# Performance work log

Hardware: AMD Instinct MI355X
Metric: run time of the kernel (lower is better)

## Reference

```python
import jax, jax.numpy as jnp
import numpy as np

D_MODEL = 1024
NUM_HEADS = 16
DEPTH = D_MODEL // NUM_HEADS
B, S = 4, 1024


def setup_inputs() -> dict:
    key = jax.random.key(0)
    ks = jax.random.split(key, 12)
    sc = 1.0 / np.sqrt(D_MODEL)
    return {
        "v": jax.random.normal(ks[0], (B, S, D_MODEL), jnp.float32),
        "k": jax.random.normal(ks[1], (B, S, D_MODEL), jnp.float32),
        "q": jax.random.normal(ks[2], (B, S, D_MODEL), jnp.float32),
        "mask": jnp.zeros((B, 1, 1, S), jnp.float32),
        "adjoin_matrix": jax.random.normal(ks[3], (B, 1, S, S), jnp.float32),
        "wq_w": jax.random.normal(ks[4], (D_MODEL, D_MODEL), jnp.float32) * sc,
        "wq_b": jnp.zeros((D_MODEL,), jnp.float32),
        "wk_w": jax.random.normal(ks[5], (D_MODEL, D_MODEL), jnp.float32) * sc,
        "wk_b": jnp.zeros((D_MODEL,), jnp.float32),
        "wv_w": jax.random.normal(ks[6], (D_MODEL, D_MODEL), jnp.float32) * sc,
        "wv_b": jnp.zeros((D_MODEL,), jnp.float32),
        "dense_w": jax.random.normal(ks[7], (D_MODEL, D_MODEL), jnp.float32) * sc,
        "dense_b": jnp.zeros((D_MODEL,), jnp.float32),
    }


def _split_heads(x, batch):
    # [B, S, D] -> [B, H, S, depth]
    return x.reshape(batch, -1, NUM_HEADS, DEPTH).transpose(0, 2, 1, 3)


def reference(v, k, q, mask, adjoin_matrix,
              wq_w, wq_b, wk_w, wk_b, wv_w, wv_b, dense_w, dense_b):
    batch = q.shape[0]
    # torch nn.Linear: y = x @ W^T + b
    qh = _split_heads(q @ wq_w.T + wq_b, batch)
    kh = _split_heads(k @ wk_w.T + wk_b, batch)
    vh = _split_heads(v @ wv_w.T + wv_b, batch)

    logits = jnp.einsum('bhqd,bhkd->bhqk', qh, kh) / jnp.sqrt(
        jnp.asarray(DEPTH, qh.dtype))
    logits = logits + mask * (-1e9) + adjoin_matrix
    attn = jax.nn.softmax(logits, axis=-1).astype(qh.dtype)
    # dropout p=0 -> identity at inference
    ctx = jnp.einsum('bhqk,bhkd->bhqd', attn, vh)  # [B,H,S,depth]
    concat = ctx.transpose(0, 2, 1, 3).reshape(batch, -1, D_MODEL)
    out = concat @ dense_w.T + dense_b
    return out, attn
```

## Files before the change

kernel.cpp:

```cpp
#include <hip/hip_runtime.h>
#include <hip/hip_bf16.h>
#include <cstdint>
#include <cstddef>

#define B_ 4
#define S_ 1024
#define D_ 1024
#define H_ 16
#define DEPTH_ 64
#define M_ (B_*S_)

typedef __attribute__((ext_vector_type(4))) float f32x4;
typedef __attribute__((ext_vector_type(8))) __bf16 bf16x8;
typedef __attribute__((ext_vector_type(8))) unsigned short u16x8;
typedef __attribute__((ext_vector_type(4))) unsigned short u16x4;

typedef const __attribute__((address_space(1))) unsigned int GU32;
typedef __attribute__((address_space(3))) unsigned int LU32;

__device__ __forceinline__ unsigned short f2bf(float f) {
  unsigned int u = __builtin_bit_cast(unsigned int, f);
  u += 0x7FFFu + ((u >> 16) & 1u);
  return (unsigned short)(u >> 16);
}

__device__ __forceinline__ float bf2f(unsigned short v) {
  unsigned int u = (unsigned int)v << 16;
  return __builtin_bit_cast(float, u);
}

struct CvtAll { const float* s[7]; unsigned short* d[7]; };

__device__ __forceinline__ void cvt_body(const float* __restrict__ s,
                                         unsigned short* __restrict__ d, int i) {
  const f32x4* sp = (const f32x4*)s + (size_t)i * 2;
  f32x4 a = sp[0], b = sp[1];
  u16x8 o;
  o[0]=f2bf(a[0]); o[1]=f2bf(a[1]); o[2]=f2bf(a[2]); o[3]=f2bf(a[3]);
  o[4]=f2bf(b[0]); o[5]=f2bf(b[1]); o[6]=f2bf(b[2]); o[7]=f2bf(b[3]);
  *((u16x8*)d + i) = o;
}

__global__ void cvt_all_kernel(CvtAll a) {
  int bi = blockIdx.x, seg, i;
  if (bi < 6144) { seg = bi >> 11;              i = ((bi & 2047) << 8) + threadIdx.x; }
  else           { int t = bi - 6144; seg = 3 + (t >> 9); i = ((t & 511) << 8) + threadIdx.x; }
  cvt_body(a.s[seg], a.d[seg], i);
}

__device__ __forceinline__ void gemm_body(
    const unsigned short* __restrict__ A,
    const unsigned short* __restrict__ Bm,
    unsigned short* __restrict__ Obf,
    float* __restrict__ Of32,
    const float* __restrict__ bias,
    int N, int K, float scale, int biasRow, int m0, int n0)
{
  __shared__ unsigned short As[128*32];
  __shared__ unsigned short Bs[128*32];
  const int tid  = threadIdx.x;
  const int lane = tid & 63;
  const int w    = tid >> 6;
  const int wm   = w >> 1, wn = w & 1;
  const int fr   = lane & 15, kg = lane >> 4;

  f32x4 acc[4][4];
  #pragma unroll
  for (int i = 0; i < 4; ++i)
    #pragma unroll
    for (int j = 0; j < 4; ++j)
      acc[i][j] = (f32x4)0.0f;

  const int o0 = tid * 16,        o1 = (256 + tid) * 16;
  const int r0 = o0 >> 6,         c0 = (o0 & 63) >> 1;
  const int r1 = o1 >> 6,         c1 = (o1 & 63) >> 1;
  const int lds0 = (w * 64) * 16;
  const int lds1 = (256 + w * 64) * 16;

  const int nkt = K >> 5;
  for (int kt = 0; kt < nkt; ++kt) {
    const int kk = kt * 32;
    __builtin_amdgcn_global_load_lds((GU32*)(A  + (size_t)(m0 + r0) * K + kk + c0),
                                     (LU32*)((char*)As + lds0), 16, 0, 0);
    __builtin_amdgcn_global_load_lds((GU32*)(A  + (size_t)(m0 + r1) * K + kk + c1),
                                     (LU32*)((char*)As + lds1), 16, 0, 0);
    __builtin_amdgcn_global_load_lds((GU32*)(Bm + (size_t)(n0 + r0) * K + kk + c0),
                                     (LU32*)((char*)Bs + lds0), 16, 0, 0);
    __builtin_amdgcn_global_load_lds((GU32*)(Bm + (size_t)(n0 + r1) * K + kk + c1),
                                     (LU32*)((char*)Bs + lds1), 16, 0, 0);
    __syncthreads();

    bf16x8 af[4], bf[4];
    #pragma unroll
    for (int i = 0; i < 4; ++i)
      af[i] = *(const bf16x8*)&As[(wm * 64 + i * 16 + fr) * 32 + kg * 8];
    #pragma unroll
    for (int j = 0; j < 4; ++j)
      bf[j] = *(const bf16x8*)&Bs[(wn * 64 + j * 16 + fr) * 32 + kg * 8];
    #pragma unroll
    for (int i = 0; i < 4; ++i)
      #pragma unroll
      for (int j = 0; j < 4; ++j)
        acc[i][j] = __builtin_amdgcn_mfma_f32_16x16x32_bf16(af[i], bf[j], acc[i][j], 0, 0, 0);
    __syncthreads();
  }

  #pragma unroll
  for (int i = 0; i < 4; ++i) {
    const int rowb = m0 + wm * 64 + i * 16 + kg * 4;
    #pragma unroll
    for (int j = 0; j < 4; ++j) {
      const int col = n0 + wn * 64 + j * 16 + fr;
      const float bcol = biasRow ? 0.0f : bias[col];
      #pragma unroll
      for (int r = 0; r < 4; ++r) {
        const int row = rowb + r;
        const float bv = biasRow ? bias[row] : bcol;
        const float val = (acc[i][j][r] + bv) * scale;
        if (Obf) Obf[(size_t)row * N + col] = f2bf(val);
        else     Of32[(size_t)row * N + col] = val;
      }
    }
  }
}

struct GemmSet { const unsigned short* A; const unsigned short* Bm;
                 unsigned short* O; const float* bias; };

__launch_bounds__(256)
__global__ void qkv_gemm(GemmSet s0, GemmSet s1, GemmSet s2) {
  const int z = blockIdx.y;
  GemmSet s = (z == 0) ? s0 : (z == 1) ? s1 : s2;
  int m0, n0, N; float scale; int biasRow;
  if (z < 2) { m0 = (blockIdx.x & 31) * 128; n0 = (blockIdx.x >> 5) * 128;
               N = D_; scale = (z == 0) ? 0.125f : 1.0f; biasRow = 0; }
  else       { m0 = (blockIdx.x & 7) * 128;  n0 = (blockIdx.x >> 3) * 128;
               N = M_; scale = 1.0f; biasRow = 1; }
  gemm_body(s.A, s.Bm, s.O, nullptr, s.bias, N, D_, scale, biasRow, m0, n0);
}

__launch_bounds__(256)
__global__ void dense_gemm(const unsigned short* __restrict__ A,
                           const unsigned short* __restrict__ Bm,
                           float* __restrict__ O, const float* __restrict__ bias) {
  gemm_body(A, Bm, nullptr, O, bias, D_, D_, 1.0f, 0,
            blockIdx.x * 128, blockIdx.y * 128);
}

__launch_bounds__(512, 2)
__global__ void attn_kernel(const unsigned short* __restrict__ qp,
                            const unsigned short* __restrict__ kp,
                            const unsigned short* __restrict__ vt,
                            const float* __restrict__ mask,
                            const float* __restrict__ adjoin,
                            float* __restrict__ attn_out,
                            unsigned short* __restrict__ ctx)
{
  __shared__ __align__(16) char L[136192];
  char* const Pb  = L;
  char* const Mbb = L + 65536;
  float* const ssum = (float*)(L + 69632);

  const int tid = threadIdx.x, lane = tid & 63, w = tid >> 6;
  const int fr = lane & 15, kg = lane >> 4;
  const int fm = w >> 2, fd = w & 3;
  const int frsw = (fr & 7) << 4;
  const int r8 = lane >> 3;
  const int c7p = (((lane & 7) ^ r8) << 4);

  char* const Wb  = L + 70656 + w * 8192;
  char* const Ks0 = Wb,        * const Ks1 = Wb + 2048;
  char* const As0 = Wb + 4096, * const As1 = Wb + 6144;

  const int i_ = blockIdx.x;
  const int bh = (i_ & 7) * 8 + ((i_ >> 3) & 7);
  const int qt = i_ >> 6;
  const int b = bh >> 4, h = bh & 15;
  const int q0 = qt * 32;
  const int kw = w * 128;

  const char* kG = (const char*)(kp + (size_t)b * S_ * D_ + h * DEPTH_);
  const char* aG = (const char*)(adjoin + (size_t)b * S_ * S_ + (size_t)q0 * S_);
  const char* vG = (const char*)(vt + (size_t)h * DEPTH_ * M_ + (size_t)b * S_);
  const char* mG = (const char*)(mask + (size_t)b * S_);

  auto stageK = [&](int t, char* dst) {
    #pragma unroll
    for (int j = 0; j < 2; ++j)
      __builtin_amdgcn_global_load_lds(
          (GU32*)(kG + (size_t)(kw + t * 16 + j * 8 + r8) * 2048 + c7p),
          (LU32*)(dst + j * 1024 + lane * 16), 16, 0, 0);
  };
  auto stageA = [&](int t, char* dst) {
    #pragma unroll
    for (int j = 0; j < 2; ++j) {
      const int qA = j * 8 + r8 + ((c7p >> 6) << 4);
      __builtin_amdgcn_global_load_lds(
          (GU32*)(aG + (size_t)qA * 4096 + kw * 4 + t * 64 + (c7p & 63)),
          (LU32*)(dst + j * 1024 + lane * 16), 16, 0, 0);
    }
  };
  auto stageV = [&](int t, char* dst) {
    #pragma unroll
    for (int j = 0; j < 2; ++j)
      __builtin_amdgcn_global_load_lds(
          (GU32*)(vG + (size_t)(fd * 16 + j * 8 + r8) * 8192 + t * 128 + c7p),
          (LU32*)(dst + j * 1024 + lane * 16), 16, 0, 0);
  };

  const unsigned short* q0p = qp + ((size_t)b * S_ + q0 + fr) * D_ + h * DEPTH_;
  const unsigned short* q1p = q0p + 16 * D_;
  bf16x8 qf00 = *(const bf16x8*)&q0p[kg * 8];
  bf16x8 qf01 = *(const bf16x8*)&q0p[32 + kg * 8];
  bf16x8 qf10 = *(const bf16x8*)&q1p[kg * 8];
  bf16x8 qf11 = *(const bf16x8*)&q1p[32 + kg * 8];

  if (w < 4)
    __builtin_amdgcn_global_load_lds((GU32*)(mG + (w << 10) + lane * 16),
                                     (LU32*)(Mbb + (w << 10) + lane * 16), 16, 0, 0);
  stageK(0, Ks0); stageA(0, As0);
  stageK(1, Ks1); stageA(1, As1);
  asm volatile("s_waitcnt vmcnt(4)" ::: "memory");
  __builtin_amdgcn_s_barrier();
  __builtin_amdgcn_sched_barrier(0);

  float ls0 = 0.0f, ls1 = 0.0f;

  #pragma unroll
  for (int t = 0; t < 8; ++t) {
    if (t == 7) asm volatile("s_waitcnt vmcnt(2)" ::: "memory");
    else        asm volatile("s_waitcnt vmcnt(4)" ::: "memory");
    __builtin_amdgcn_sched_barrier(0);

    const char* kb = (t & 1) ? Ks1 : Ks0;
    const char* ab = (t & 1) ? As1 : As0;
    bf16x8 kf0 = *(const bf16x8*)(kb + fr * 128 + ((kg * 16) ^ frsw));
    bf16x8 kf1 = *(const bf16x8*)(kb + fr * 128 + ((64 + kg * 16) ^ frsw));
    f32x4 a40 = *(const f32x4*)(ab + fr * 128 + ((kg * 16) ^ frsw));
    f32x4 a41 = *(const f32x4*)(ab + fr * 128 + ((64 + kg * 16) ^ frsw));
    f32x4 m4  = *(const f32x4*)(Mbb + kw * 4 + t * 64 + kg * 16);

    asm volatile("s_waitcnt lgkmcnt(0)" ::: "memory");
    __builtin_amdgcn_sched_barrier(0);

    if (t < 6)      { stageK(t + 2, (t & 1) ? Ks1 : Ks0);
                      stageA(t + 2, (t & 1) ? As1 : As0); }
    else if (t == 6)  stageV(0, As0);
    else              stageV(1, As1);

    f32x4 s0 = (f32x4)0.0f, s1 = (f32x4)0.0f;
    s0 = __builtin_amdgcn_mfma_f32_16x16x32_bf16(kf0, qf00, s0, 0, 0, 0);
    s0 = __builtin_amdgcn_mfma_f32_16x16x32_bf16(kf1, qf01, s0, 0, 0, 0);
    s1 = __builtin_amdgcn_mfma_f32_16x16x32_bf16(kf0, qf10, s1, 0, 0, 0);
    s1 = __builtin_amdgcn_mfma_f32_16x16x32_bf16(kf1, qf11, s1, 0, 0, 0);

    f32x4 p0, p1;
    #pragma unroll
    for (int r = 0; r < 4; ++r) {
      p0[r] = __expf(s0[r] + a40[r] + m4[r] * (-1e9f));
      p1[r] = __expf(s1[r] + a41[r] + m4[r] * (-1e9f));
    }
    ls0 += (p0[0] + p0[1]) + (p0[2] + p0[3]);
    ls1 += (p1[0] + p1[1]) + (p1[2] + p1[3]);
    u16x4 pk0, pk1;
    #pragma unroll
    for (int r = 0; r < 4; ++r) { pk0[r] = f2bf(p0[r]); pk1[r] = f2bf(p1[r]); }
    const int pcol = (kw * 2 + t * 32 + kg * 8) ^ frsw;
    *(u16x4*)(Pb + fr * 2048 + pcol)        = pk0;
    *(u16x4*)(Pb + (16 + fr) * 2048 + pcol) = pk1;
  }

  ls0 += __shfl_xor(ls0, 16); ls0 += __shfl_xor(ls0, 32);
  ls1 += __shfl_xor(ls1, 16); ls1 += __shfl_xor(ls1, 32);
  if (lane < 16) {
    ssum[lane * 8 + w]        = ls0;
    ssum[(16 + lane) * 8 + w] = ls1;
  }

  asm volatile("s_waitcnt lgkmcnt(0)" ::: "memory");
  __builtin_amdgcn_s_barrier();
  __builtin_amdgcn_sched_barrier(0);

  const int q = fm * 16 + fr;
  f32x4 cacc = (f32x4)0.0f;
  #pragma unroll
  for (int t = 0; t < 16; ++t) {
    if (t == 15) asm volatile("s_waitcnt vmcnt(0)" ::: "memory");
    else         asm volatile("s_waitcnt vmcnt(2)" ::: "memory");
    __builtin_amdgcn_sched_barrier(0);

    const char* vb = (t & 1) ? As1 : As0;
    bf16x8 vf0 = *(const bf16x8*)(vb + fr * 128 + ((kg * 16) ^ frsw));
    bf16x8 vf1 = *(const bf16x8*)(vb + fr * 128 + ((64 + kg * 16) ^ frsw));
    bf16x8 pf0 = *(const bf16x8*)(Pb + q * 2048 + ((t * 128 + kg * 16) ^ frsw));
    bf16x8 pf1 = *(const bf16x8*)(Pb + q * 2048 + ((t * 128 + 64 + kg * 16) ^ frsw));

    asm volatile("s_waitcnt lgkmcnt(0)" ::: "memory");
    __builtin_amdgcn_sched_barrier(0);

    if (t < 14) stageV(t + 2, (t & 1) ? As1 : As0);

    cacc = __builtin_amdgcn_mfma_f32_16x16x32_bf16(vf0, pf0, cacc, 0, 0, 0);
    cacc = __builtin_amdgcn_mfma_f32_16x16x32_bf16(vf1, pf1, cacc, 0, 0, 0);
  }

  {
    f32x4 sa = *(const f32x4*)&ssum[q * 8];
    f32x4 sb = *(const f32x4*)&ssum[q * 8 + 4];
    const float giC = 1.0f / ((sa[0] + sa[1]) + (sa[2] + sa[3]) +
                              ((sb[0] + sb[1]) + (sb[2] + sb[3])));
    u16x4 cv;
    #pragma unroll
    for (int r = 0; r < 4; ++r) cv[r] = f2bf(cacc[r] * giC);
    *(u16x4*)&ctx[((size_t)b * S_ + q0 + q) * D_ + h * DEPTH_ + fd * 16 + kg * 4] = cv;
  }

  #pragma unroll
  for (int j = 0; j < 4; ++j) {
    const int row = w * 4 + j;
    f32x4 ta = *(const f32x4*)&ssum[row * 8];
    f32x4 tb = *(const f32x4*)&ssum[row * 8 + 4];
    const float g = 1.0f / ((ta[0] + ta[1]) + (ta[2] + ta[3]) +
                            ((tb[0] + tb[1]) + (tb[2] + tb[3])));
    const char* pr = Pb + row * 2048;
    const int rs = (row & 7) << 4;
    float* ao = attn_out + ((size_t)bh * S_ + q0 + row) * S_;
    #pragma unroll
    for (int half = 0; half < 2; ++half) {
      u16x8 pv = *(const u16x8*)(pr + ((half * 1024 + lane * 16) ^ rs));
      f32x4 o0, o1;
      #pragma unroll
      for (int e = 0; e < 4; ++e) { o0[e] = bf2f(pv[e]) * g; o1[e] = bf2f(pv[4 + e]) * g; }
      __builtin_nontemporal_store(o0, (f32x4*)(ao + half * 512 + lane * 8));
      __builtin_nontemporal_store(o1, (f32x4*)(ao + half * 512 + lane * 8 + 4));
    }
  }
}

extern "C" void kernel_launch(void* const* d_in, const int* in_sizes, int n_in,
                              void* d_out, int out_size, void* d_ws, size_t ws_size,
                              hipStream_t stream)
{
  const float* v_in   = (const float*)d_in[0];
  const float* k_in   = (const float*)d_in[1];
  const float* q_in   = (const float*)d_in[2];
  const float* mask   = (const float*)d_in[3];
  const float* adjoin = (const float*)d_in[4];
  const float* wq_w   = (const float*)d_in[5];
  const float* wq_b   = (const float*)d_in[6];
  const float* wk_w   = (const float*)d_in[7];
  const float* wk_b   = (const float*)d_in[8];
  const float* wv_w   = (const float*)d_in[9];
  const float* wv_b   = (const float*)d_in[10];
  const float* wd_w   = (const float*)d_in[11];
  const float* wd_b   = (const float*)d_in[12];

  unsigned short* xq  = (unsigned short*)d_ws;
  unsigned short* xk  = xq  + (size_t)M_ * D_;
  unsigned short* xv  = xk  + (size_t)M_ * D_;
  unsigned short* wqb = xv  + (size_t)M_ * D_;
  unsigned short* wkb = wqb + (size_t)D_ * D_;
  unsigned short* wvb = wkb + (size_t)D_ * D_;
  unsigned short* wdb = wvb + (size_t)D_ * D_;
  unsigned short* qp  = wdb + (size_t)D_ * D_;
  unsigned short* kp  = qp  + (size_t)M_ * D_;
  unsigned short* vt  = kp  + (size_t)M_ * D_;
  unsigned short* ctx = vt  + (size_t)M_ * D_;

  float* out  = (float*)d_out;
  float* attn = out + (size_t)B_ * S_ * D_;

  CvtAll ca;
  ca.s[0] = q_in; ca.s[1] = k_in; ca.s[2] = v_in;
  ca.s[3] = wq_w; ca.s[4] = wk_w; ca.s[5] = wv_w; ca.s[6] = wd_w;
  ca.d[0] = xq;   ca.d[1] = xk;   ca.d[2] = xv;
  ca.d[3] = wqb;  ca.d[4] = wkb;  ca.d[5] = wvb;  ca.d[6] = wdb;
  cvt_all_kernel<<<8192, 256, 0, stream>>>(ca);

  GemmSet sq{xq,  wqb, qp, wq_b};
  GemmSet sk{xk,  wkb, kp, wk_b};
  GemmSet sv{wvb, xv,  vt, wv_b};
  qkv_gemm<<<dim3(256, 3), 256, 0, stream>>>(sq, sk, sv);

  attn_kernel<<<B_ * H_ * (S_ / 32), 512, 0, stream>>>(qp, kp, vt, mask, adjoin, attn, ctx);

  dense_gemm<<<dim3(32, 8), 256, 0, stream>>>(ctx, wdb, out, wd_b);
}
```

Measured before the change: 196.7 us.

## Halve attention query tile to 16 rows, split PV over key halves

Each attention block now handles 16 query rows instead of 32, cutting LDS from about 136KB to 80KB and raising the launch-bounds occupancy target from 2 to 4 blocks per CU. The PV stage is split across two wave groups that each cover half the keys, and their partial accumulators are summed through LDS. Mask values are kept in registers, and V tiles reuse the K buffers. The aim is to hide the memory latency of streaming adjoin and attn with more concurrent blocks, at the cost of reloading K and V twice as often per query and an extra reduction barrier.

```diff
diff --git a/kernel.cpp b/kernel.cpp
--- a/kernel.cpp
+++ b/kernel.cpp
@@ -147,7 +147,7 @@
             blockIdx.x * 128, blockIdx.y * 128);
 }
 
-__launch_bounds__(512, 2)
+__launch_bounds__(512, 4)
 __global__ void attn_kernel(const unsigned short* __restrict__ qp,
                             const unsigned short* __restrict__ kp,
                             const unsigned short* __restrict__ vt,
@@ -156,27 +156,26 @@
                             float* __restrict__ attn_out,
                             unsigned short* __restrict__ ctx)
 {
-  __shared__ __align__(16) char L[136192];
-  char* const Pb  = L;
-  char* const Mbb = L + 65536;
-  float* const ssum = (float*)(L + 69632);
+  __shared__ __align__(16) char L[81920];
+  char* const Pb = L;
+  char* const Rg = L + 32768;
 
   const int tid = threadIdx.x, lane = tid & 63, w = tid >> 6;
   const int fr = lane & 15, kg = lane >> 4;
-  const int fm = w >> 2, fd = w & 3;
+  const int fd = w & 3, kh = w >> 2;
   const int frsw = (fr & 7) << 4;
   const int r8 = lane >> 3;
   const int c7p = (((lane & 7) ^ r8) << 4);
 
-  char* const Wb  = L + 70656 + w * 8192;
+  char* const Wb  = Rg + w * 6144;
   char* const Ks0 = Wb,        * const Ks1 = Wb + 2048;
-  char* const As0 = Wb + 4096, * const As1 = Wb + 6144;
+  char* const Ab0 = Wb + 4096, * const Ab1 = Wb + 5120;
 
   const int i_ = blockIdx.x;
   const int bh = (i_ & 7) * 8 + ((i_ >> 3) & 7);
   const int qt = i_ >> 6;
   const int b = bh >> 4, h = bh & 15;
-  const int q0 = qt * 32;
+  const int q0 = qt * 16;
   const int kw = w * 128;
 
   const char* kG = (const char*)(kp + (size_t)b * S_ * D_ + h * DEPTH_);
@@ -192,136 +191,127 @@
           (LU32*)(dst + j * 1024 + lane * 16), 16, 0, 0);
   };
   auto stageA = [&](int t, char* dst) {
-    #pragma unroll
-    for (int j = 0; j < 2; ++j) {
-      const int qA = j * 8 + r8 + ((c7p >> 6) << 4);
-      __builtin_amdgcn_global_load_lds(
-          (GU32*)(aG + (size_t)qA * 4096 + kw * 4 + t * 64 + (c7p & 63)),
-          (LU32*)(dst + j * 1024 + lane * 16), 16, 0, 0);
-    }
+    __builtin_amdgcn_global_load_lds(
+        (GU32*)(aG + (size_t)(lane >> 2) * 4096 + kw * 4 + t * 64 + (lane & 3) * 16),
+        (LU32*)(dst + lane * 16), 16, 0, 0);
   };
   auto stageV = [&](int t, char* dst) {
     #pragma unroll
     for (int j = 0; j < 2; ++j)
       __builtin_amdgcn_global_load_lds(
-          (GU32*)(vG + (size_t)(fd * 16 + j * 8 + r8) * 8192 + t * 128 + c7p),
+          (GU32*)(vG + (size_t)(fd * 16 + j * 8 + r8) * 8192 + kh * 1024 + t * 128 + c7p),
           (LU32*)(dst + j * 1024 + lane * 16), 16, 0, 0);
   };
 
-  const unsigned short* q0p = qp + ((size_t)b * S_ + q0 + fr) * D_ + h * DEPTH_;
-  const unsigned short* q1p = q0p + 16 * D_;
-  bf16x8 qf00 = *(const bf16x8*)&q0p[kg * 8];
-  bf16x8 qf01 = *(const bf16x8*)&q0p[32 + kg * 8];
-  bf16x8 qf10 = *(const bf16x8*)&q1p[kg * 8];
-  bf16x8 qf11 = *(const bf16x8*)&q1p[32 + kg * 8];
-
-  if (w < 4)
-    __builtin_amdgcn_global_load_lds((GU32*)(mG + (w << 10) + lane * 16),
-                                     (LU32*)(Mbb + (w << 10) + lane * 16), 16, 0, 0);
-  stageK(0, Ks0); stageA(0, As0);
-  stageK(1, Ks1); stageA(1, As1);
-  asm volatile("s_waitcnt vmcnt(4)" ::: "memory");
-  __builtin_amdgcn_s_barrier();
+  const unsigned short* qrow = qp + ((size_t)b * S_ + q0 + fr) * D_ + h * DEPTH_;
+  bf16x8 qf0 = *(const bf16x8*)&qrow[kg * 8];
+  bf16x8 qf1 = *(const bf16x8*)&qrow[32 + kg * 8];
+  f32x4 mreg[8];
+  #pragma unroll
+  for (int t = 0; t < 8; ++t)
+    mreg[t] = *(const f32x4*)(mG + kw * 4 + t * 64 + kg * 16);
+  asm volatile("" ::: "memory");
+
+  stageK(0, Ks0); stageA(0, Ab0);
+  stageK(1, Ks1); stageA(1, Ab1);
+  asm volatile("s_waitcnt vmcnt(3)" ::: "memory");
   __builtin_amdgcn_sched_barrier(0);
 
-  float ls0 = 0.0f, ls1 = 0.0f;
+  float ls = 0.0f;
 
   #pragma unroll
   for (int t = 0; t < 8; ++t) {
-    if (t == 7) asm volatile("s_waitcnt vmcnt(2)" ::: "memory");
-    else        asm volatile("s_waitcnt vmcnt(4)" ::: "memory");
+    if (t == 7)     asm volatile("s_waitcnt vmcnt(2)" ::: "memory");
+    else if (t > 0) asm volatile("s_waitcnt vmcnt(3)" ::: "memory");
     __builtin_amdgcn_sched_barrier(0);
 
     const char* kb = (t & 1) ? Ks1 : Ks0;
-    const char* ab = (t & 1) ? As1 : As0;
+    const char* ab = (t & 1) ? Ab1 : Ab0;
     bf16x8 kf0 = *(const bf16x8*)(kb + fr * 128 + ((kg * 16) ^ frsw));
     bf16x8 kf1 = *(const bf16x8*)(kb + fr * 128 + ((64 + kg * 16) ^ frsw));
-    f32x4 a40 = *(const f32x4*)(ab + fr * 128 + ((kg * 16) ^ frsw));
-    f32x4 a41 = *(const f32x4*)(ab + fr * 128 + ((64 + kg * 16) ^ frsw));
-    f32x4 m4  = *(const f32x4*)(Mbb + kw * 4 + t * 64 + kg * 16);
+    f32x4 a4  = *(const f32x4*)(ab + fr * 64 + kg * 16);
 
     asm volatile("s_waitcnt lgkmcnt(0)" ::: "memory");
     __builtin_amdgcn_sched_barrier(0);
 
     if (t < 6)      { stageK(t + 2, (t & 1) ? Ks1 : Ks0);
-                      stageA(t + 2, (t & 1) ? As1 : As0); }
-    else if (t == 6)  stageV(0, As0);
-    else              stageV(1, As1);
-
-    f32x4 s0 = (f32x4)0.0f, s1 = (f32x4)0.0f;
-    s0 = __builtin_amdgcn_mfma_f32_16x16x32_bf16(kf0, qf00, s0, 0, 0, 0);
-    s0 = __builtin_amdgcn_mfma_f32_16x16x32_bf16(kf1, qf01, s0, 0, 0, 0);
-    s1 = __builtin_amdgcn_mfma_f32_16x16x32_bf16(kf0, qf10, s1, 0, 0, 0);
-    s1 = __builtin_amdgcn_mfma_f32_16x16x32_bf16(kf1, qf11, s1, 0, 0, 0);
-
-    f32x4 p0, p1;
-    #pragma unroll
-    for (int r = 0; r < 4; ++r) {
-      p0[r] = __expf(s0[r] + a40[r] + m4[r] * (-1e9f));
-      p1[r] = __expf(s1[r] + a41[r] + m4[r] * (-1e9f));
-    }
-    ls0 += (p0[0] + p0[1]) + (p0[2] + p0[3]);
-    ls1 += (p1[0] + p1[1]) + (p1[2] + p1[3]);
-    u16x4 pk0, pk1;
-    #pragma unroll
-    for (int r = 0; r < 4; ++r) { pk0[r] = f2bf(p0[r]); pk1[r] = f2bf(p1[r]); }
-    const int pcol = (kw * 2 + t * 32 + kg * 8) ^ frsw;
-    *(u16x4*)(Pb + fr * 2048 + pcol)        = pk0;
-    *(u16x4*)(Pb + (16 + fr) * 2048 + pcol) = pk1;
-  }
-
-  ls0 += __shfl_xor(ls0, 16); ls0 += __shfl_xor(ls0, 32);
-  ls1 += __shfl_xor(ls1, 16); ls1 += __shfl_xor(ls1, 32);
-  if (lane < 16) {
-    ssum[lane * 8 + w]        = ls0;
-    ssum[(16 + lane) * 8 + w] = ls1;
-  }
+                      stageA(t + 2, (t & 1) ? Ab1 : Ab0); }
+    else if (t == 6)  stageV(0, Ks0);
+    else              stageV(1, Ks1);
+
+    f32x4 s = (f32x4)0.0f;
+    s = __builtin_amdgcn_mfma_f32_16x16x32_bf16(kf0, qf0, s, 0, 0, 0);
+    s = __builtin_amdgcn_mfma_f32_16x16x32_bf16(kf1, qf1, s, 0, 0, 0);
+
+    f32x4 p;
+    #pragma unroll
+    for (int r = 0; r < 4; ++r)
+      p[r] = __expf(s[r] + a4[r] + mreg[t][r] * (-1e9f));
+    ls += (p[0] + p[1]) + (p[2] + p[3]);
+    u16x4 pk;
+    #pragma unroll
+    for (int r = 0; r < 4; ++r) pk[r] = f2bf(p[r]);
+    *(u16x4*)(Pb + fr * 2048 + ((kw * 2 + t * 32 + kg * 8) ^ frsw)) = pk;
+  }
+
+  ls += __shfl_xor(ls, 16);
+  ls += __shfl_xor(ls, 32);
+  if (lane < 16) *(float*)(Ab0 + lane * 4) = ls;
 
   asm volatile("s_waitcnt lgkmcnt(0)" ::: "memory");
   __builtin_amdgcn_s_barrier();
   __builtin_amdgcn_sched_barrier(0);
 
-  const int q = fm * 16 + fr;
   f32x4 cacc = (f32x4)0.0f;
   #pragma unroll
-  for (int t = 0; t < 16; ++t) {
-    if (t == 15) asm volatile("s_waitcnt vmcnt(0)" ::: "memory");
-    else         asm volatile("s_waitcnt vmcnt(2)" ::: "memory");
+  for (int t = 0; t < 8; ++t) {
+    if (t == 7) asm volatile("s_waitcnt vmcnt(0)" ::: "memory");
+    else        asm volatile("s_waitcnt vmcnt(2)" ::: "memory");
     __builtin_amdgcn_sched_barrier(0);
 
-    const char* vb = (t & 1) ? As1 : As0;
+    const char* vb = (t & 1) ? Ks1 : Ks0;
     bf16x8 vf0 = *(const bf16x8*)(vb + fr * 128 + ((kg * 16) ^ frsw));
     bf16x8 vf1 = *(const bf16x8*)(vb + fr * 128 + ((64 + kg * 16) ^ frsw));
-    bf16x8 pf0 = *(const bf16x8*)(Pb + q * 2048 + ((t * 128 + kg * 16) ^ frsw));
-    bf16x8 pf1 = *(const bf16x8*)(Pb + q * 2048 + ((t * 128 + 64 + kg * 16) ^ frsw));
+    bf16x8 pf0 = *(const bf16x8*)(Pb + fr * 2048 + ((kh * 1024 + t * 128 + kg * 16) ^ frsw));
+    bf16x8 pf1 = *(const bf16x8*)(Pb + fr * 2048 + ((kh * 1024 + t * 128 + 64 + kg * 16) ^ frsw));
 
     asm volatile("s_waitcnt lgkmcnt(0)" ::: "memory");
     __builtin_amdgcn_sched_barrier(0);
 
-    if (t < 14) stageV(t + 2, (t & 1) ? As1 : As0);
+    if (t < 6) stageV(t + 2, (t & 1) ? Ks1 : Ks0);
 
     cacc = __builtin_amdgcn_mfma_f32_16x16x32_bf16(vf0, pf0, cacc, 0, 0, 0);
     cacc = __builtin_amdgcn_mfma_f32_16x16x32_bf16(vf1, pf1, cacc, 0, 0, 0);
   }
 
-  {
-    f32x4 sa = *(const f32x4*)&ssum[q * 8];
-    f32x4 sb = *(const f32x4*)&ssum[q * 8 + 4];
-    const float giC = 1.0f / ((sa[0] + sa[1]) + (sa[2] + sa[3]) +
-                              ((sb[0] + sb[1]) + (sb[2] + sb[3])));
+  if (w >= 4) *(f32x4*)(Ab1 + lane * 16) = cacc;
+  asm volatile("s_waitcnt lgkmcnt(0)" ::: "memory");
+  __builtin_amdgcn_s_barrier();
+  __builtin_amdgcn_sched_barrier(0);
+
+  if (w < 4) {
+    f32x4 red = *(const f32x4*)(Rg + (w + 4) * 6144 + 5120 + lane * 16);
+    #pragma unroll
+    for (int r = 0; r < 4; ++r) cacc[r] += red[r];
+    float gs = 0.0f;
+    #pragma unroll
+    for (int w2 = 0; w2 < 8; ++w2)
+      gs += *(const float*)(Rg + w2 * 6144 + 4096 + fr * 4);
+    const float giC = 1.0f / gs;
     u16x4 cv;
     #pragma unroll
     for (int r = 0; r < 4; ++r) cv[r] = f2bf(cacc[r] * giC);
-    *(u16x4*)&ctx[((size_t)b * S_ + q0 + q) * D_ + h * DEPTH_ + fd * 16 + kg * 4] = cv;
-  }
-
-  #pragma unroll
-  for (int j = 0; j < 4; ++j) {
-    const int row = w * 4 + j;
-    f32x4 ta = *(const f32x4*)&ssum[row * 8];
-    f32x4 tb = *(const f32x4*)&ssum[row * 8 + 4];
-    const float g = 1.0f / ((ta[0] + ta[1]) + (ta[2] + ta[3]) +
-                            ((tb[0] + tb[1]) + (tb[2] + tb[3])));
+    *(u16x4*)&ctx[((size_t)b * S_ + q0 + fr) * D_ + h * DEPTH_ + fd * 16 + kg * 4] = cv;
+  }
+
+  #pragma unroll
+  for (int j = 0; j < 2; ++j) {
+    const int row = w * 2 + j;
+    float gs = 0.0f;
+    #pragma unroll
+    for (int w2 = 0; w2 < 8; ++w2)
+      gs += *(const float*)(Rg + w2 * 6144 + 4096 + row * 4);
+    const float g = 1.0f / gs;
     const char* pr = Pb + row * 2048;
     const int rs = (row & 7) << 4;
     float* ao = attn_out + ((size_t)bh * S_ + q0 + row) * S_;
@@ -382,7 +372,7 @@
   GemmSet sv{wvb, xv,  vt, wv_b};
   qkv_gemm<<<dim3(256, 3), 256, 0, stream>>>(sq, sk, sv);
 
-  attn_kernel<<<B_ * H_ * (S_ / 32), 512, 0, stream>>>(qp, kp, vt, mask, adjoin, attn, ctx);
+  attn_kernel<<<B_ * H_ * (S_ / 16), 512, 0, stream>>>(qp, kp, vt, mask, adjoin, attn, ctx);
 
   dense_gemm<<<dim3(32, 8), 256, 0, stream>>>(ctx, wdb, out, wd_b);
 }
```

After: 186.8 us (median of 2 runs). 1.05x faster.
